# Kernel optimization log

Measured on AMD Instinct MI355X. Metric: run time of the kernel, lower is better.

Reference implementation:

```python
import jax, jax.numpy as jnp
from jax import lax
import numpy as np

# Module hyperparameters (init_kwargs)
NITERS = 10
NROWS, NCOLS = 16, 16
NSUP = NROWS * NCOLS
COMPACT = 10.0
CONST = 100.0
NCONV = 10  # stage1_nconv; also nfeat of imfeat and shifter_size
B, H, W = 2, 512, 512

DN = ('NCHW', 'OIHW', 'NCHW')


def conv2d(x, w, b=None):
    y = lax.conv_general_dilated(x, w, (1, 1), 'SAME', dimension_numbers=DN)
    return y if b is None else y + b[None, :, None, None]


def blockmean(x):
    # adaptive_avg_pool2d to (NROWS, NCOLS); H,W chosen divisible -> exact block mean
    Bz, C, Hx, Wx = x.shape
    return x.reshape(Bz, C, NROWS, Hx // NROWS, NCOLS, Wx // NCOLS).mean((3, 5))


def box3(x):
    # 3x3 all-ones depthwise conv with zero padding (the "shifter" conv)
    C = x.shape[1]
    k = jnp.ones((C, 1, 3, 3), x.dtype)
    return lax.conv_general_dilated(x, k, (1, 1), 'SAME', feature_group_count=C,
                                    dimension_numbers=DN)


def setup_inputs() -> dict:
    key = jax.random.key(0)
    ks = jax.random.split(key, 7)
    s = 0.15  # ~He init for 3x3 convs with ~10 channels; keeps activations O(1)
    return {
        'X': jax.random.normal(ks[0], (B, 3, H, W), jnp.float32),
        'w0': jax.random.normal(ks[1], (NCONV, 3, 3, 3), jnp.float32) * s,
        'b0': jax.random.normal(ks[2], (NCONV,), jnp.float32) * s,
        'ws_mid': jax.random.normal(ks[3], (NCONV - 2, NCONV, NCONV, 3, 3), jnp.float32) * s,
        'bs_mid': jax.random.normal(ks[4], (NCONV - 2, NCONV), jnp.float32) * s,
        'wf': jax.random.normal(ks[5], (NCONV - 5, NCONV, 3, 3), jnp.float32) * s,
        'bf': jax.random.normal(ks[6], (NCONV - 5,), jnp.float32) * s,
    }


def _forward(X, w0, b0, ws_mid, bs_mid, wf, bf):
    Bz, _, Hx, Wx = X.shape
    h = jax.nn.relu(conv2d(X, w0, b0))

    def layer(hc, wb):
        w, b = wb
        return jax.nn.relu(conv2d(hc, w, b)), None

    h, _ = lax.scan(layer, h, (ws_mid, bs_mid))
    s1 = conv2d(h, wf, bf)  # B x (NCONV-5) x H x W

    # ---- imfeat = [stage1, X, Xgrid, Ygrid] -> B x NCONV x H x W ----
    Yg, Xg = jnp.meshgrid(jnp.arange(Hx, dtype=X.dtype), jnp.arange(Wx, dtype=X.dtype),
                          indexing='ij')
    imfeat = jnp.concatenate([
        s1, X,
        jnp.broadcast_to(Xg, (Bz, 1, Hx, Wx)),
        jnp.broadcast_to(Yg, (Bz, 1, Hx, Wx)),
    ], axis=1)
    C = imfeat.shape[1]

    # ckern: ones, except spatial (last two) channels weighted by compactness scale
    ck = jnp.ones((C,), imfeat.dtype).at[-2:].set(
        jnp.asarray(COMPACT / np.sqrt(Hx * Wx / NSUP), imfeat.dtype))

    # pixel -> parent superpixel indices (nearest-neighbor upsample of coarse grid)
    Yc = jnp.arange(Hx) * NROWS // Hx  # (H,)
    Xc = jnp.arange(Wx) * NCOLS // Wx  # (W,)
    shifts = [(dr, dc) for dr in (-1, 0, 1) for dc in (-1, 0, 1)]
    Y1 = jnp.stack([jnp.clip(Yc + dr, 0, NROWS - 1) for dr, _ in shifts])[:, :, None]  # (9,H,1)
    X1 = jnp.stack([jnp.clip(Xc + dc, 0, NCOLS - 1) for _, dc in shifts])[:, None, :]  # (9,1,W)

    def affinity_fn(cent):
        cup = cent[:, :, Y1, X1]
        d = (imfeat[:, :, None] - cup) * ck[None, :, None, None, None]
        return jnp.exp(-(d * d).mean(1) / CONST)

    def centroids_fn(aff):
        # sum over the 9 shifts commutes with block-mean and the shared 3x3 box conv
        asum = aff.sum(1, keepdims=True)
        num = box3(blockmean(imfeat * asum))  # B x C x NROWS x NCOLS
        den = box3(blockmean(asum))
        return num / den

    cent0 = blockmean(imfeat)
    aff0 = affinity_fn(cent0)

    @jax.checkpoint
    def step(carry, _):
        cent, _a = carry
        aff = affinity_fn(cent)
        return (centroids_fn(aff), aff), None

    (cent, aff), _ = lax.scan(step, (cent0, aff0), None, length=NITERS)
    # returned affinity corresponds to centroids before the last update (as in torch)
    return cent, aff


def reference(X, w0, b0, ws_mid, bs_mid, wf, bf):
    return _forward(X, w0, b0, ws_mid, bs_mid, wf, bf)
```

## Files before the change

### kernel.cpp

```cpp
#include <hip/hip_runtime.h>

#define HH 512
#define WW 512
#define BB 2
#define CKXY 0.3125f
#define HW (HH*WW)

typedef short bf16x8 __attribute__((ext_vector_type(8)));
typedef float f32x4  __attribute__((ext_vector_type(4)));

__device__ __forceinline__ unsigned short f2bf(float f) {
  unsigned u = __float_as_uint(f);
  u += 0x7FFF + ((u >> 16) & 1);
  return (unsigned short)(u >> 16);
}
__device__ __forceinline__ unsigned pack2(float lo, float hi) {
  return (unsigned)f2bf(lo) | ((unsigned)f2bf(hi) << 16);
}

template<int CIN, bool BF16IN, bool RELU>
__global__ __launch_bounds__(512) void conv_mfma_u(const void* __restrict__ in,
    const float* __restrict__ w, const float* __restrict__ bias,
    unsigned* __restrict__ outu) {
  const int bx = blockIdx.x, by = blockIdx.y, b = blockIdx.z;
  const int tid = threadIdx.x;
  const int gy0 = by * 32, gx0 = bx * 32;
  __shared__ unsigned short sT[34 * 34 * 16];

  const int lane = tid & 63;
  const int g = lane >> 4;
  const int co = lane & 15;
  bf16x8 Bf[5];
  #pragma unroll
  for (int P = 0; P < 5; ++P) {
    #pragma unroll
    for (int j = 0; j < 8; ++j) {
      const int tap = 2 * P + (g >> 1);
      const int ci = ((g & 1) << 3) + j;
      unsigned short v = 0;
      if (co < 10 && ci < CIN && tap < 9)
        v = f2bf(w[(co * CIN + ci) * 9 + tap]);
      Bf[P][j] = (short)v;
    }
  }
  const float bs = (co < 10) ? bias[co] : 0.f;

  for (int p = tid; p < 34 * 34; p += 512) {
    const int ly = p / 34, lx = p - ly * 34;
    const int gy = gy0 + ly - 1, gx = gx0 + lx - 1;
    const bool ok = ((unsigned)gy < HH) && ((unsigned)gx < WW);
    const int pix = gy * WW + gx;
    unsigned u[8];
    if (BF16IN) {
      const unsigned* pp = (const unsigned*)in + (size_t)b * 5 * HW + pix;
      #pragma unroll
      for (int c2 = 0; c2 < 8; ++c2)
        u[c2] = (c2 < (CIN + 1) / 2 && ok) ? pp[c2 * HW] : 0u;
    } else {
      const float* pp = (const float*)in + (size_t)b * CIN * HW + pix;
      #pragma unroll
      for (int c2 = 0; c2 < 8; ++c2) {
        float f0 = (2 * c2 < CIN && ok) ? pp[(2 * c2) * HW] : 0.f;
        float f1 = (2 * c2 + 1 < CIN && ok) ? pp[(2 * c2 + 1) * HW] : 0.f;
        u[c2] = pack2(f0, f1);
      }
    }
    uint4* dst = reinterpret_cast<uint4*>(&sT[p * 16]);
    dst[0] = make_uint4(u[0], u[1], u[2], u[3]);
    dst[1] = make_uint4(u[4], u[5], u[6], u[7]);
  }
  __syncthreads();

  const int wave = tid >> 6;
  unsigned* ob = outu + (size_t)b * 5 * HW;
  for (int i = 0; i < 8; ++i) {
    const int t = wave * 8 + i;
    const int py = t >> 1;
    const int pxb = (t & 1) << 4;
    f32x4 acc = {bs, bs, bs, bs};
    #pragma unroll
    for (int P = 0; P < 5; ++P) {
      int tap = 2 * P + (g >> 1);
      if (tap > 8) tap = 8;
      const int dy = tap / 3 - 1, dx = tap % 3 - 1;
      const int m = lane & 15;
      const int addr = ((py + 1 + dy) * 34 + (pxb + m + 1 + dx)) * 16 + ((g & 1) << 3);
      bf16x8 a = *reinterpret_cast<const bf16x8*>(&sT[addr]);
      acc = __builtin_amdgcn_mfma_f32_16x16x32_bf16(a, Bf[P], acc, 0, 0, 0);
    }
    float o0 = acc[0], o1 = acc[1], o2 = acc[2], o3 = acc[3];
    if (RELU) { o0 = fmaxf(o0, 0.f); o1 = fmaxf(o1, 0.f); o2 = fmaxf(o2, 0.f); o3 = fmaxf(o3, 0.f); }
    const float q0 = __shfl_xor(o0, 1), q1 = __shfl_xor(o1, 1);
    const float q2 = __shfl_xor(o2, 1), q3 = __shfl_xor(o3, 1);
    if (!(co & 1) && co < 10) {
      const int y = gy0 + py;
      const int x = gx0 + pxb + (g << 2);
      uint4 st;
      st.x = pack2(o0, q0); st.y = pack2(o1, q1);
      st.z = pack2(o2, q2); st.w = pack2(o3, q3);
      *reinterpret_cast<uint4*>(&ob[(co >> 1) * HW + y * WW + x]) = st;
    }
  }
}

__global__ __launch_bounds__(512) void conv_final_mfma(const unsigned* __restrict__ in,
    const float* __restrict__ w, const float* __restrict__ bias,
    const float* __restrict__ X, float* __restrict__ imfeat,
    float* __restrict__ cent0) {
  const int bx = blockIdx.x, by = blockIdx.y, b = blockIdx.z;
  const int tid = threadIdx.x;
  const int gy0 = by * 32, gx0 = bx * 32;
  __shared__ unsigned short sT[34 * 34 * 16];
  __shared__ float sC[8][5];
  __shared__ float sX[8][3];

  const int lane = tid & 63;
  const int g = lane >> 4;
  const int co = lane & 15;
  bf16x8 Bf[5];
  #pragma unroll
  for (int P = 0; P < 5; ++P) {
    #pragma unroll
    for (int j = 0; j < 8; ++j) {
      const int tap = 2 * P + (g >> 1);
      const int ci = ((g & 1) << 3) + j;
      unsigned short v = 0;
      if (co < 5 && ci < 10 && tap < 9)
        v = f2bf(w[(co * 10 + ci) * 9 + tap]);
      Bf[P][j] = (short)v;
    }
  }
  const float bs = (co < 5) ? bias[co] : 0.f;

  for (int p = tid; p < 34 * 34; p += 512) {
    const int ly = p / 34, lx = p - ly * 34;
    const int gy = gy0 + ly - 1, gx = gx0 + lx - 1;
    const bool ok = ((unsigned)gy < HH) && ((unsigned)gx < WW);
    const unsigned* pp = in + (size_t)b * 5 * HW + gy * WW + gx;
    unsigned u[5];
    #pragma unroll
    for (int c2 = 0; c2 < 5; ++c2) u[c2] = ok ? pp[c2 * HW] : 0u;
    uint4* dst = reinterpret_cast<uint4*>(&sT[p * 16]);
    dst[0] = make_uint4(u[0], u[1], u[2], u[3]);
    dst[1] = make_uint4(u[4], 0u, 0u, 0u);
  }
  __syncthreads();

  const int wave = tid >> 6;
  float* ob = imfeat + (size_t)b * 10 * HW;
  float cSum = 0.f;
  for (int i = 0; i < 8; ++i) {
    const int t = wave * 8 + i;
    const int py = t >> 1;
    const int pxb = (t & 1) << 4;
    f32x4 acc = {bs, bs, bs, bs};
    #pragma unroll
    for (int P = 0; P < 5; ++P) {
      int tap = 2 * P + (g >> 1);
      if (tap > 8) tap = 8;
      const int dy = tap / 3 - 1, dx = tap % 3 - 1;
      const int m = lane & 15;
      const int addr = ((py + 1 + dy) * 34 + (pxb + m + 1 + dx)) * 16 + ((g & 1) << 3);
      bf16x8 a = *reinterpret_cast<const bf16x8*>(&sT[addr]);
      acc = __builtin_amdgcn_mfma_f32_16x16x32_bf16(a, Bf[P], acc, 0, 0, 0);
    }
    if (co < 5) {
      const int y = gy0 + py;
      const int x = gx0 + pxb + (g << 2);
      float4 o; o.x = acc[0]; o.y = acc[1]; o.z = acc[2]; o.w = acc[3];
      *reinterpret_cast<float4*>(&ob[co * HW + y * WW + x]) = o;
    }
    cSum += acc[0] + acc[1] + acc[2] + acc[3];
  }
  cSum += __shfl_xor(cSum, 16);
  cSum += __shfl_xor(cSum, 32);
  if (lane < 5) sC[wave][lane] = cSum;

  const float* Xb = X + (size_t)b * 3 * HW;
  float xs[3] = {0.f, 0.f, 0.f};
  for (int p = tid; p < 1024; p += 512) {
    const int y = gy0 + (p >> 5), x = gx0 + (p & 31);
    const int pix = y * WW + x;
    #pragma unroll
    for (int c = 0; c < 3; ++c) {
      float v = Xb[c * HW + pix];
      ob[(5 + c) * HW + pix] = v;
      xs[c] += v;
    }
    ob[8 * HW + pix] = (float)x * CKXY;
    ob[9 * HW + pix] = (float)y * CKXY;
  }
  #pragma unroll
  for (int off = 32; off; off >>= 1) {
    #pragma unroll
    for (int c = 0; c < 3; ++c) xs[c] += __shfl_down(xs[c], off);
  }
  if (lane == 0) {
    #pragma unroll
    for (int c = 0; c < 3; ++c) sX[wave][c] = xs[c];
  }
  __syncthreads();
  if (tid < 5) {
    float s = 0.f;
    #pragma unroll
    for (int wv = 0; wv < 8; ++wv) s += sC[wv][tid];
    cent0[((b * 10 + tid) * 16 + by) * 16 + bx] = s * (1.0f / 1024.0f);
  }
  if (tid >= 64 && tid < 67) {
    const int c = tid - 64;
    float s = 0.f;
    #pragma unroll
    for (int wv = 0; wv < 8; ++wv) s += sX[wv][c];
    cent0[((b * 10 + 5 + c) * 16 + by) * 16 + bx] = s * (1.0f / 1024.0f);
  }
  if (tid == 128) cent0[((b * 10 + 8) * 16 + by) * 16 + bx] = ((float)gx0 + 15.5f) * CKXY;
  if (tid == 129) cent0[((b * 10 + 9) * 16 + by) * 16 + bx] = ((float)gy0 + 15.5f) * CKXY;
}

__global__ __launch_bounds__(256) void iter2(const float* __restrict__ imfeat,
    const float* __restrict__ centIn, const float* __restrict__ numP,
    const float* __restrict__ denP, float* __restrict__ numO,
    float* __restrict__ denO, float* __restrict__ affO) {
  const int cx = blockIdx.x, cy = blockIdx.y, b = blockIdx.z;
  const int tid = threadIdx.x;
  __shared__ float sc[9][10];
  __shared__ float nb[9][11];
  if (centIn) {
    if (tid < 90) {
      int s = tid / 10, ch = tid - s * 10;
      int dr = s / 3 - 1, dc = s % 3 - 1;
      int r = min(max(cy + dr, 0), 15), c = min(max(cx + dc, 0), 15);
      sc[s][ch] = centIn[((b * 10 + ch) * 16 + r) * 16 + c];
    }
    __syncthreads();
  } else {
    if (tid < 99) {
      int s = tid / 11, j = tid - s * 11;
      int dr = s / 3 - 1, dc = s % 3 - 1;
      int r = min(max(cy + dr, 0), 15), c = min(max(cx + dc, 0), 15);
      float a = 0.f;
      #pragma unroll
      for (int rr = -1; rr <= 1; ++rr)
        #pragma unroll
        for (int cc = -1; cc <= 1; ++cc) {
          int R = r + rr, C = c + cc;
          if ((unsigned)R < 16u && (unsigned)C < 16u)
            a += (j < 10) ? numP[((b * 10 + j) * 16 + R) * 16 + C]
                          : denP[(b * 16 + R) * 16 + C];
        }
      nb[s][j] = a;
    }
    __syncthreads();
    if (tid < 90) {
      int s = tid / 10, ch = tid - s * 10;
      sc[s][ch] = nb[s][ch] / nb[s][10];
    }
    __syncthreads();
  }

  float accN[10];
  #pragma unroll
  for (int ch = 0; ch < 10; ++ch) accN[ch] = 0.f;
  float accD = 0.f;
  const int col = tid & 31, row0 = tid >> 5;
  for (int p = 0; p < 4; ++p) {
    const int y = cy * 32 + row0 + p * 8;
    const int x = cx * 32 + col;
    float f[10];
    #pragma unroll
    for (int ch = 0; ch < 10; ++ch)
      f[ch] = imfeat[((b * 10 + ch) * HH + y) * WW + x];
    float asum = 0.f;
    #pragma unroll
    for (int s = 0; s < 9; ++s) {
      float ss = 0.f;
      #pragma unroll
      for (int ch = 0; ch < 10; ++ch) { float d = f[ch] - sc[s][ch]; ss = fmaf(d, d, ss); }
      float a = __expf(-ss * (1.0f / 1000.0f));
      asum += a;
      if (affO) affO[((b * 9 + s) * HH + y) * WW + x] = a;
    }
    accD += asum;
    #pragma unroll
    for (int ch = 0; ch < 10; ++ch) accN[ch] = fmaf(f[ch], asum, accN[ch]);
  }
  #pragma unroll
  for (int off = 32; off; off >>= 1) {
    accD += __shfl_down(accD, off);
    #pragma unroll
    for (int ch = 0; ch < 10; ++ch) accN[ch] += __shfl_down(accN[ch], off);
  }
  __shared__ float sPart[4][11];
  const int wave = tid >> 6, lane = tid & 63;
  if (lane == 0) {
    #pragma unroll
    for (int ch = 0; ch < 10; ++ch) sPart[wave][ch] = accN[ch];
    sPart[wave][10] = accD;
  }
  __syncthreads();
  if (tid < 11) {
    float s = sPart[0][tid] + sPart[1][tid] + sPart[2][tid] + sPart[3][tid];
    if (tid < 10) numO[((b * 10 + tid) * 16 + cy) * 16 + cx] = s;
    else denO[(b * 16 + cy) * 16 + cx] = s;
  }
}

__global__ __launch_bounds__(256) void cent_final(const float* __restrict__ num_bs,
    const float* __restrict__ den_bs, float* __restrict__ out_cent) {
  const int b = blockIdx.x;
  const int tid = threadIdx.x;
  const int cy = tid >> 4, cx = tid & 15;
  float den = 0.f;
  #pragma unroll
  for (int dr = -1; dr <= 1; ++dr)
    #pragma unroll
    for (int dc = -1; dc <= 1; ++dc) {
      int r = cy + dr, c = cx + dc;
      if ((unsigned)r < 16 && (unsigned)c < 16) den += den_bs[(b * 16 + r) * 16 + c];
    }
  #pragma unroll
  for (int ch = 0; ch < 10; ++ch) {
    float num = 0.f;
    #pragma unroll
    for (int dr = -1; dr <= 1; ++dr)
      #pragma unroll
      for (int dc = -1; dc <= 1; ++dc) {
        int r = cy + dr, c = cx + dc;
        if ((unsigned)r < 16 && (unsigned)c < 16)
          num += num_bs[((b * 10 + ch) * 16 + r) * 16 + c];
      }
    float invck = (ch >= 8) ? (1.0f / CKXY) : 1.0f;
    out_cent[((b * 10 + ch) * 16 + cy) * 16 + cx] = (num / den) * invck;
  }
}

extern "C" void kernel_launch(void* const* d_in, const int* in_sizes, int n_in,
                              void* d_out, int out_size, void* d_ws, size_t ws_size,
                              hipStream_t stream) {
  const float* X      = (const float*)d_in[0];
  const float* w0     = (const float*)d_in[1];
  const float* b0     = (const float*)d_in[2];
  const float* ws_mid = (const float*)d_in[3];
  const float* bs_mid = (const float*)d_in[4];
  const float* wf     = (const float*)d_in[5];
  const float* bf     = (const float*)d_in[6];
  float* out = (float*)d_out;

  const size_t uplane = (size_t)BB * 5 * HW;
  unsigned* uA   = (unsigned*)d_ws;
  unsigned* uB   = uA + uplane;
  float* imfeat  = (float*)(uB + uplane);
  float* num0    = imfeat + (size_t)BB * 10 * HW;
  float* den0    = num0 + BB * 10 * 256;
  float* num1    = den0 + BB * 256;
  float* den1    = num1 + BB * 10 * 256;
  float* centA   = den1 + BB * 256;

  dim3 cgrid(16, 16, BB);
  conv_mfma_u<3, false, true><<<cgrid, 512, 0, stream>>>(X, w0, b0, uA);
  const unsigned* cur = uA;
  unsigned* nxt = uB;
  for (int l = 0; l < 8; ++l) {
    conv_mfma_u<10, true, true><<<cgrid, 512, 0, stream>>>(cur, ws_mid + l * 900, bs_mid + l * 10, nxt);
    const unsigned* t = cur; cur = nxt; nxt = (unsigned*)t;
  }
  conv_final_mfma<<<cgrid, 512, 0, stream>>>(cur, wf, bf, X, imfeat, centA);

  float* aff_out = out + BB * 10 * 256;
  float* nums[2] = {num0, num1};
  float* dens[2] = {den0, den1};
  for (int k = 0; k < 10; ++k) {
    iter2<<<cgrid, 256, 0, stream>>>(imfeat,
        (k == 0) ? centA : nullptr,
        (k == 0) ? nullptr : nums[(k - 1) & 1],
        (k == 0) ? nullptr : dens[(k - 1) & 1],
        nums[k & 1], dens[k & 1],
        (k == 9) ? aff_out : nullptr);
  }
  cent_final<<<dim3(BB), 256, 0, stream>>>(nums[1], dens[1], out);
}
```

Baseline: 255.7 us.

## Store imfeat as packed bf16 and halve conv tile height

The imfeat feature map that the ten iteration kernels read is now stored as packed bf16 pairs (5 planes) instead of 10 fp32 planes. This halves the bytes each iteration reads and the bytes the final conv writes. The mid conv kernels also use 32x16 tiles with twice as many blocks, giving more blocks across the CUs at the cost of more halo reloads. Rounding the features and coordinates to bf16 adds error to the affinity and centroid outputs.

Result: slower. 306.1 us (+19.7%).

```diff
diff --git a/kernel.cpp b/kernel.cpp
--- a/kernel.cpp
+++ b/kernel.cpp
@@ -18,14 +18,14 @@
   return (unsigned)f2bf(lo) | ((unsigned)f2bf(hi) << 16);
 }
 
-template<int CIN, bool BF16IN, bool RELU>
+template<int CIN, bool BF16IN>
 __global__ __launch_bounds__(512) void conv_mfma_u(const void* __restrict__ in,
     const float* __restrict__ w, const float* __restrict__ bias,
     unsigned* __restrict__ outu) {
   const int bx = blockIdx.x, by = blockIdx.y, b = blockIdx.z;
   const int tid = threadIdx.x;
-  const int gy0 = by * 32, gx0 = bx * 32;
-  __shared__ unsigned short sT[34 * 34 * 16];
+  const int gy0 = by * 16, gx0 = bx * 32;
+  __shared__ unsigned short sT[18 * 34 * 16];
 
   const int lane = tid & 63;
   const int g = lane >> 4;
@@ -45,7 +45,7 @@
   }
   const float bs = (co < 10) ? bias[co] : 0.f;
 
-  for (int p = tid; p < 34 * 34; p += 512) {
+  for (int p = tid; p < 18 * 34; p += 512) {
     const int ly = p / 34, lx = p - ly * 34;
     const int gy = gy0 + ly - 1, gx = gx0 + lx - 1;
     const bool ok = ((unsigned)gy < HH) && ((unsigned)gx < WW);
@@ -73,8 +73,8 @@
 
   const int wave = tid >> 6;
   unsigned* ob = outu + (size_t)b * 5 * HW;
-  for (int i = 0; i < 8; ++i) {
-    const int t = wave * 8 + i;
+  for (int i = 0; i < 4; ++i) {
+    const int t = wave * 4 + i;
     const int py = t >> 1;
     const int pxb = (t & 1) << 4;
     f32x4 acc = {bs, bs, bs, bs};
@@ -88,8 +88,8 @@
       bf16x8 a = *reinterpret_cast<const bf16x8*>(&sT[addr]);
       acc = __builtin_amdgcn_mfma_f32_16x16x32_bf16(a, Bf[P], acc, 0, 0, 0);
     }
-    float o0 = acc[0], o1 = acc[1], o2 = acc[2], o3 = acc[3];
-    if (RELU) { o0 = fmaxf(o0, 0.f); o1 = fmaxf(o1, 0.f); o2 = fmaxf(o2, 0.f); o3 = fmaxf(o3, 0.f); }
+    float o0 = fmaxf(acc[0], 0.f), o1 = fmaxf(acc[1], 0.f);
+    float o2 = fmaxf(acc[2], 0.f), o3 = fmaxf(acc[3], 0.f);
     const float q0 = __shfl_xor(o0, 1), q1 = __shfl_xor(o1, 1);
     const float q2 = __shfl_xor(o2, 1), q3 = __shfl_xor(o3, 1);
     if (!(co & 1) && co < 10) {
@@ -105,7 +105,7 @@
 
 __global__ __launch_bounds__(512) void conv_final_mfma(const unsigned* __restrict__ in,
     const float* __restrict__ w, const float* __restrict__ bias,
-    const float* __restrict__ X, float* __restrict__ imfeat,
+    const float* __restrict__ X, unsigned* __restrict__ imfeat,
     float* __restrict__ cent0) {
   const int bx = blockIdx.x, by = blockIdx.y, b = blockIdx.z;
   const int tid = threadIdx.x;
@@ -147,7 +147,8 @@
   __syncthreads();
 
   const int wave = tid >> 6;
-  float* ob = imfeat + (size_t)b * 10 * HW;
+  unsigned* ob = imfeat + (size_t)b * 5 * HW;
+  const float* Xb = X + (size_t)b * 3 * HW;
   float cSum = 0.f;
   for (int i = 0; i < 8; ++i) {
     const int t = wave * 8 + i;
@@ -164,11 +165,21 @@
       bf16x8 a = *reinterpret_cast<const bf16x8*>(&sT[addr]);
       acc = __builtin_amdgcn_mfma_f32_16x16x32_bf16(a, Bf[P], acc, 0, 0, 0);
     }
-    if (co < 5) {
-      const int y = gy0 + py;
-      const int x = gx0 + pxb + (g << 2);
-      float4 o; o.x = acc[0]; o.y = acc[1]; o.z = acc[2]; o.w = acc[3];
-      *reinterpret_cast<float4*>(&ob[co * HW + y * WW + x]) = o;
+    const int y = gy0 + py;
+    const int x = gx0 + pxb + (g << 2);
+    const float q0 = __shfl_xor(acc[0], 1), q1 = __shfl_xor(acc[1], 1);
+    const float q2 = __shfl_xor(acc[2], 1), q3 = __shfl_xor(acc[3], 1);
+    if (co == 0 || co == 2) {
+      uint4 st;
+      st.x = pack2(acc[0], q0); st.y = pack2(acc[1], q1);
+      st.z = pack2(acc[2], q2); st.w = pack2(acc[3], q3);
+      *reinterpret_cast<uint4*>(&ob[(co >> 1) * HW + y * WW + x]) = st;
+    } else if (co == 4) {
+      float4 xv = *reinterpret_cast<const float4*>(&Xb[y * WW + x]);
+      uint4 st;
+      st.x = pack2(acc[0], xv.x); st.y = pack2(acc[1], xv.y);
+      st.z = pack2(acc[2], xv.z); st.w = pack2(acc[3], xv.w);
+      *reinterpret_cast<uint4*>(&ob[2 * HW + y * WW + x]) = st;
     }
     cSum += acc[0] + acc[1] + acc[2] + acc[3];
   }
@@ -176,19 +187,16 @@
   cSum += __shfl_xor(cSum, 32);
   if (lane < 5) sC[wave][lane] = cSum;
 
-  const float* Xb = X + (size_t)b * 3 * HW;
   float xs[3] = {0.f, 0.f, 0.f};
   for (int p = tid; p < 1024; p += 512) {
     const int y = gy0 + (p >> 5), x = gx0 + (p & 31);
     const int pix = y * WW + x;
-    #pragma unroll
-    for (int c = 0; c < 3; ++c) {
-      float v = Xb[c * HW + pix];
-      ob[(5 + c) * HW + pix] = v;
-      xs[c] += v;
-    }
-    ob[8 * HW + pix] = (float)x * CKXY;
-    ob[9 * HW + pix] = (float)y * CKXY;
+    float x0 = Xb[pix];
+    float x1 = Xb[HW + pix];
+    float x2 = Xb[2 * HW + pix];
+    xs[0] += x0; xs[1] += x1; xs[2] += x2;
+    ob[3 * HW + pix] = pack2(x1, x2);
+    ob[4 * HW + pix] = pack2((float)x * CKXY, (float)y * CKXY);
   }
   #pragma unroll
   for (int off = 32; off; off >>= 1) {
@@ -217,7 +225,7 @@
   if (tid == 129) cent0[((b * 10 + 9) * 16 + by) * 16 + bx] = ((float)gy0 + 15.5f) * CKXY;
 }
 
-__global__ __launch_bounds__(256) void iter2(const float* __restrict__ imfeat,
+__global__ __launch_bounds__(256) void iter2(const unsigned* __restrict__ imfeat,
     const float* __restrict__ centIn, const float* __restrict__ numP,
     const float* __restrict__ denP, float* __restrict__ numO,
     float* __restrict__ denO, float* __restrict__ affO) {
@@ -266,10 +274,14 @@
   for (int p = 0; p < 4; ++p) {
     const int y = cy * 32 + row0 + p * 8;
     const int x = cx * 32 + col;
+    const unsigned* fb = imfeat + (size_t)b * 5 * HW + y * WW + x;
     float f[10];
     #pragma unroll
-    for (int ch = 0; ch < 10; ++ch)
-      f[ch] = imfeat[((b * 10 + ch) * HH + y) * WW + x];
+    for (int c2 = 0; c2 < 5; ++c2) {
+      unsigned u = fb[c2 * HW];
+      f[2 * c2]     = __uint_as_float(u << 16);
+      f[2 * c2 + 1] = __uint_as_float(u & 0xFFFF0000u);
+    }
     float asum = 0.f;
     #pragma unroll
     for (int s = 0; s < 9; ++s) {
@@ -347,30 +359,31 @@
   float* out = (float*)d_out;
 
   const size_t uplane = (size_t)BB * 5 * HW;
-  unsigned* uA   = (unsigned*)d_ws;
-  unsigned* uB   = uA + uplane;
-  float* imfeat  = (float*)(uB + uplane);
-  float* num0    = imfeat + (size_t)BB * 10 * HW;
-  float* den0    = num0 + BB * 10 * 256;
-  float* num1    = den0 + BB * 256;
-  float* den1    = num1 + BB * 10 * 256;
-  float* centA   = den1 + BB * 256;
-
-  dim3 cgrid(16, 16, BB);
-  conv_mfma_u<3, false, true><<<cgrid, 512, 0, stream>>>(X, w0, b0, uA);
+  unsigned* uA     = (unsigned*)d_ws;
+  unsigned* uB     = uA + uplane;
+  unsigned* imfeat = uB + uplane;
+  float* num0      = (float*)(imfeat + uplane);
+  float* den0      = num0 + BB * 10 * 256;
+  float* num1      = den0 + BB * 256;
+  float* den1      = num1 + BB * 10 * 256;
+  float* centA     = den1 + BB * 256;
+
+  dim3 cgrid(16, 32, BB);
+  conv_mfma_u<3, false><<<cgrid, 512, 0, stream>>>(X, w0, b0, uA);
   const unsigned* cur = uA;
   unsigned* nxt = uB;
   for (int l = 0; l < 8; ++l) {
-    conv_mfma_u<10, true, true><<<cgrid, 512, 0, stream>>>(cur, ws_mid + l * 900, bs_mid + l * 10, nxt);
+    conv_mfma_u<10, true><<<cgrid, 512, 0, stream>>>(cur, ws_mid + l * 900, bs_mid + l * 10, nxt);
     const unsigned* t = cur; cur = nxt; nxt = (unsigned*)t;
   }
-  conv_final_mfma<<<cgrid, 512, 0, stream>>>(cur, wf, bf, X, imfeat, centA);
+  dim3 fgrid(16, 16, BB);
+  conv_final_mfma<<<fgrid, 512, 0, stream>>>(cur, wf, bf, X, imfeat, centA);
 
   float* aff_out = out + BB * 10 * 256;
   float* nums[2] = {num0, num1};
   float* dens[2] = {den0, den1};
   for (int k = 0; k < 10; ++k) {
-    iter2<<<cgrid, 256, 0, stream>>>(imfeat,
+    iter2<<<fgrid, 256, 0, stream>>>(imfeat,
         (k == 0) ? centA : nullptr,
         (k == 0) ? nullptr : nums[(k - 1) & 1],
         (k == 0) ? nullptr : dens[(k - 1) & 1],
```
